# Optimization experiments

Measured on AMD Instinct MI355X. Metric: run time of the kernel, lower is better.

The kernel has to match this reference:

```python
import jax, jax.numpy as jnp
import numpy as np

SUB1 = 0.5
SUB2 = 0.2


def setup_inputs() -> dict:
    key = jax.random.key(0)
    k1, k2, k3 = jax.random.split(key, 3)
    x = jax.random.normal(k1, (32, 64, 128, 128), dtype=jnp.float32)
    conv_weight = jax.random.normal(k2, (128, 64, 3, 3), dtype=jnp.float32) * 0.05
    conv_bias = jax.random.normal(k3, (128,), dtype=jnp.float32) * 0.05
    return {"x": x, "conv_weight": conv_weight, "conv_bias": conv_bias}


def reference(x, conv_weight, conv_bias):
    # Conv2d, stride 1, VALID padding (kernel computes out_h = in_h - K + 1)
    y = jax.lax.conv_general_dilated(
        x, conv_weight,
        window_strides=(1, 1), padding="VALID",
        dimension_numbers=("NCHW", "OIHW", "NCHW"))
    y = y + conv_bias[None, :, None, None]
    v = y - SUB1 - SUB2
    # Mish: v * tanh(softplus(v)); softplus == log(1 + exp(v)) (stable form)
    return v * jnp.tanh(jax.nn.softplus(v))
```

## Files before the change

### kernel.cpp

```cpp
#include <hip/hip_runtime.h>
#include <hip/hip_bf16.h>

typedef short bf16x8 __attribute__((ext_vector_type(8)));
typedef float f32x4 __attribute__((ext_vector_type(4)));

constexpr int C_IN = 64, H_IN = 128, W_IN = 128, C_OUT = 128, OH = 126, OW = 126;
constexpr int PAD = 72;
constexpr float SUBC = 0.7f;

__global__ void reorder_weights(const float* __restrict__ w, __hip_bfloat16* __restrict__ wr) {
    int o = blockIdx.x * 256 + threadIdx.x;
    if (o >= 9 * C_OUT * C_IN) return;
    int ci = o & 63;
    int co = (o >> 6) & 127;
    int k9 = o >> 13;
    int kh = k9 / 3, kw = k9 % 3;
    wr[o] = __float2bfloat16(w[((co * C_IN + ci) * 3 + kh) * 3 + kw]);
}

__global__ __launch_bounds__(256, 2) void conv_mish(
    const float* __restrict__ x, const __hip_bfloat16* __restrict__ wr,
    const float* __restrict__ bias, float* __restrict__ out)
{
    __shared__ __hip_bfloat16 Xs[128 * PAD];
    __shared__ __hip_bfloat16 Bs[128 * PAD];

    int b = blockIdx.x;
    int lb = (b & 7) * 504 + (b >> 3);
    int n  = lb / OH;
    int oh = lb % OH;

    int tid  = threadIdx.x;
    int lane = tid & 63;
    int wv   = tid >> 6;
    int wm   = wv >> 1;
    int wn   = wv & 1;
    int quad = lane >> 4;
    int l16  = lane & 15;

    f32x4 acc[4][4] = {};

    const float* xn = x + (size_t)n * C_IN * H_IN * W_IN;

    for (int kh = 0; kh < 3; ++kh) {
        __syncthreads();
        {
            int h   = oh + kh;
            int w4  = (tid & 31) * 4;
            int cib = tid >> 5;
            for (int r = 0; r < 8; ++r) {
                int ci = cib + r * 8;
                float4 v = *(const float4*)(xn + ((size_t)ci * H_IN + h) * W_IN + w4);
                Xs[(w4 + 0) * PAD + ci] = __float2bfloat16(v.x);
                Xs[(w4 + 1) * PAD + ci] = __float2bfloat16(v.y);
                Xs[(w4 + 2) * PAD + ci] = __float2bfloat16(v.z);
                Xs[(w4 + 3) * PAD + ci] = __float2bfloat16(v.w);
            }
        }
        for (int kw = 0; kw < 3; ++kw) {
            if (kw) __syncthreads();
            {
                const __hip_bfloat16* src = wr + ((kh * 3 + kw) << 13);
                for (int r = 0; r < 4; ++r) {
                    int c   = tid + r * 256;
                    int co  = c >> 3;
                    int ci8 = (c & 7) << 3;
                    *(bf16x8*)&Bs[co * PAD + ci8] = *(const bf16x8*)(src + co * 64 + ci8);
                }
            }
            __syncthreads();
            for (int half = 0; half < 2; ++half) {
                int k0 = half * 32 + quad * 8;
                bf16x8 a[4], bf[4];
                for (int i = 0; i < 4; ++i) {
                    int m = wm * 64 + i * 16 + l16;
                    int widx = m + kw; if (widx > 127) widx = 127;
                    a[i] = *(const bf16x8*)&Xs[widx * PAD + k0];
                }
                for (int j = 0; j < 4; ++j) {
                    int co = wn * 64 + j * 16 + l16;
                    bf[j] = *(const bf16x8*)&Bs[co * PAD + k0];
                }
                for (int i = 0; i < 4; ++i)
                    for (int j = 0; j < 4; ++j)
                        acc[i][j] = __builtin_amdgcn_mfma_f32_16x16x32_bf16(a[i], bf[j], acc[i][j], 0, 0, 0);
            }
        }
    }

    for (int j = 0; j < 4; ++j) {
        int co = wn * 64 + j * 16 + l16;
        float bb = bias[co] - SUBC;
        for (int i = 0; i < 4; ++i) {
            int ow0 = wm * 64 + i * 16 + quad * 4;
            float o[4];
            for (int r = 0; r < 4; ++r) {
                float v = acc[i][j][r] + bb;
                float e = __expf(v);
                float t = e * (e + 2.0f);
                float m = v * t * __builtin_amdgcn_rcpf(t + 2.0f);
                o[r] = (v > 20.0f) ? v : m;
            }
            float* dst = out + (((size_t)n * C_OUT + co) * OH + oh) * OW + ow0;
            float2 p0; p0.x = o[0]; p0.y = o[1];
            *(float2*)dst = p0;
            if (ow0 + 2 < OW) {
                float2 p1; p1.x = o[2]; p1.y = o[3];
                *(float2*)(dst + 2) = p1;
            }
        }
    }
}

extern "C" void kernel_launch(void* const* d_in, const int* in_sizes, int n_in,
                              void* d_out, int out_size, void* d_ws, size_t ws_size,
                              hipStream_t stream) {
    const float* x    = (const float*)d_in[0];
    const float* w    = (const float*)d_in[1];
    const float* bias = (const float*)d_in[2];
    float* out        = (float*)d_out;
    __hip_bfloat16* wr = (__hip_bfloat16*)d_ws;

    reorder_weights<<<(9 * C_OUT * C_IN + 255) / 256, 256, 0, stream>>>(w, wr);
    conv_mish<<<32 * OH, 256, 0, stream>>>(x, wr, bias, out);
}
```

Measured before the change: 450.5 us.

## Load weights directly from global, drop weight LDS tile, raise occupancy

Removes the shared-memory staging of the per-tap weight tile and has each wave read its bf16 weight fragments straight from global/L2, which eliminates two barriers per kw step. It also rewrites the input staging so each thread gathers 8 channels for one column and writes a single 16-byte vector to LDS instead of four scalar bf16 stores. Halving LDS use lets launch bounds request 4 blocks per SM. The cost is more global/L2 weight traffic per block and tighter register limits, which could cause spills with 64 accumulator floats.

Result: slower. 564.8 us (+25.4%).

```diff
diff --git a/kernel.cpp b/kernel.cpp
--- a/kernel.cpp
+++ b/kernel.cpp
@@ -18,12 +18,11 @@
     wr[o] = __float2bfloat16(w[((co * C_IN + ci) * 3 + kh) * 3 + kw]);
 }
 
-__global__ __launch_bounds__(256, 2) void conv_mish(
+__global__ __launch_bounds__(256, 4) void conv_mish(
     const float* __restrict__ x, const __hip_bfloat16* __restrict__ wr,
     const float* __restrict__ bias, float* __restrict__ out)
 {
     __shared__ __hip_bfloat16 Xs[128 * PAD];
-    __shared__ __hip_bfloat16 Bs[128 * PAD];
 
     int b = blockIdx.x;
     int lb = (b & 7) * 504 + (b >> 3);
@@ -45,43 +44,41 @@
     for (int kh = 0; kh < 3; ++kh) {
         __syncthreads();
         {
-            int h   = oh + kh;
-            int w4  = (tid & 31) * 4;
-            int cib = tid >> 5;
-            for (int r = 0; r < 8; ++r) {
-                int ci = cib + r * 8;
-                float4 v = *(const float4*)(xn + ((size_t)ci * H_IN + h) * W_IN + w4);
-                Xs[(w4 + 0) * PAD + ci] = __float2bfloat16(v.x);
-                Xs[(w4 + 1) * PAD + ci] = __float2bfloat16(v.y);
-                Xs[(w4 + 2) * PAD + ci] = __float2bfloat16(v.z);
-                Xs[(w4 + 3) * PAD + ci] = __float2bfloat16(v.w);
+            int h = oh + kh;
+            for (int r = 0; r < 4; ++r) {
+                int t  = tid + r * 256;
+                int w  = t & 127;
+                int cb = t >> 7;
+                const float* gp = xn + ((size_t)(cb * 8) * H_IN + h) * W_IN + w;
+                alignas(16) __hip_bfloat16 tmp[8];
+                #pragma unroll
+                for (int e = 0; e < 8; ++e)
+                    tmp[e] = __float2bfloat16(gp[(size_t)e * (H_IN * W_IN)]);
+                *(bf16x8*)&Xs[w * PAD + cb * 8] = *(const bf16x8*)tmp;
             }
         }
+        __syncthreads();
+
         for (int kw = 0; kw < 3; ++kw) {
-            if (kw) __syncthreads();
-            {
-                const __hip_bfloat16* src = wr + ((kh * 3 + kw) << 13);
-                for (int r = 0; r < 4; ++r) {
-                    int c   = tid + r * 256;
-                    int co  = c >> 3;
-                    int ci8 = (c & 7) << 3;
-                    *(bf16x8*)&Bs[co * PAD + ci8] = *(const bf16x8*)(src + co * 64 + ci8);
-                }
-            }
-            __syncthreads();
+            const __hip_bfloat16* src = wr + ((kh * 3 + kw) << 13);
+            #pragma unroll
             for (int half = 0; half < 2; ++half) {
                 int k0 = half * 32 + quad * 8;
                 bf16x8 a[4], bf[4];
+                #pragma unroll
+                for (int j = 0; j < 4; ++j) {
+                    int co = wn * 64 + j * 16 + l16;
+                    bf[j] = *(const bf16x8*)(src + co * 64 + k0);
+                }
+                #pragma unroll
                 for (int i = 0; i < 4; ++i) {
                     int m = wm * 64 + i * 16 + l16;
                     int widx = m + kw; if (widx > 127) widx = 127;
                     a[i] = *(const bf16x8*)&Xs[widx * PAD + k0];
                 }
-                for (int j = 0; j < 4; ++j) {
-                    int co = wn * 64 + j * 16 + l16;
-                    bf[j] = *(const bf16x8*)&Bs[co * PAD + k0];
-                }
+                #pragma unroll
                 for (int i = 0; i < 4; ++i)
+                    #pragma unroll
                     for (int j = 0; j < 4; ++j)
                         acc[i][j] = __builtin_amdgcn_mfma_f32_16x16x32_bf16(a[i], bf[j], acc[i][j], 0, 0, 0);
             }
```
